# Kernel tuning notes

Measured on AMD Instinct MI355X. Metric: run time of the kernel, lower is better.

Reference implementation:

```python
import jax, jax.numpy as jnp
import numpy as np

B = 1024      # number of samples (sample_idx.shape[0])
H = 256       # hidden_size
E = 64        # number of observation events
NO = 512      # observed samples per event
D = 16        # input_size
ND = 2        # n_dim
S = 4         # euler ODE steps between consecutive events
EPS = 1e-8


def setup_inputs() -> dict:
    key = jax.random.key(0)
    ks = jax.random.split(key, 24)
    X = jax.random.normal(ks[0], (E, NO, D, ND), jnp.float32)
    M = jnp.ones((E, NO, D), jnp.float32)
    rng = np.random.default_rng(0)
    # distinct indices per event (torch scatter temp[i_obs]=... assumes no dup within event)
    batch_idx = jnp.asarray(
        np.stack([rng.permutation(B)[:NO] for _ in range(E)]).astype(np.int32))
    dt = jnp.float32(0.05)
    s = 1.0 / np.sqrt(H)
    def U(k, shp):
        return jax.random.uniform(k, shp, jnp.float32, -s, s)
    inp = {"X": X, "M": M, "batch_idx": batch_idx, "dt": dt}
    # GRU-ODE cell (3 Linear layers H->H, bias init 0.01 in torch; random here)
    inp["ode_Wr"], inp["ode_br"] = U(ks[1], (H, H)), U(ks[2], (H,))
    inp["ode_Wz"], inp["ode_bz"] = U(ks[3], (H, H)), U(ks[4], (H,))
    inp["ode_Wh"], inp["ode_bh"] = U(ks[5], (H, H)), U(ks[6], (H,))
    # GRUCell for observation update: input size 2*D, hidden H
    inp["g_Wxr"], inp["g_Wxz"], inp["g_Wxn"] = U(ks[7], (2 * D, H)), U(ks[8], (2 * D, H)), U(ks[9], (2 * D, H))
    inp["g_Uhr"], inp["g_Uhz"], inp["g_Uhn"] = U(ks[10], (H, H)), U(ks[11], (H, H)), U(ks[12], (H, H))
    inp["g_bxr"], inp["g_bxz"], inp["g_bxn"] = U(ks[13], (H,)), U(ks[14], (H,)), U(ks[15], (H,))
    inp["g_bhr"], inp["g_bhz"], inp["g_bhn"] = U(ks[16], (H,)), U(ks[17], (H,)), U(ks[18], (H,))
    # p_model: Linear(H,H) -> ReLU -> (Dropout p=0, identity in eval) -> Linear(H, D-1)
    inp["p_W1"], inp["p_b1"] = U(ks[19], (H, H)), U(ks[20], (H,))
    inp["p_W2"], inp["p_b2"] = U(ks[21], (H, D - 1)), U(ks[22], (D - 1,))
    return inp


def reference(X, M, batch_idx, dt,
              ode_Wr, ode_br, ode_Wz, ode_bz, ode_Wh, ode_bh,
              g_Wxr, g_Wxz, g_Wxn, g_Uhr, g_Uhz, g_Uhn,
              g_bxr, g_bxz, g_bxn, g_bhr, g_bhz, g_bhn,
              p_W1, p_b1, p_W2, p_b2):
    def euler_step(h):
        r = jax.nn.sigmoid(h @ ode_Wr + ode_br)
        z = jax.nn.sigmoid(h @ ode_Wz + ode_bz)
        u = jnp.tanh((r * h) @ ode_Wh + ode_bh)
        return h + dt * (1.0 - z) * (u - h)

    def event_step(carry, xs):
        h, mse, mae, mape, tot = carry
        Xe, Me, ie = xs                      # [NO,D,ND], [NO,D], [NO]
        for _ in range(S):                   # ODE evolution up to this obs time
            h = euler_step(h)
        p = jax.nn.relu(h @ p_W1 + p_b1) @ p_W2 + p_b2   # [B, D-1]
        Xt = Xe[:, 1:, 0]                    # X_obs[:, :, 0][:, 1:]
        Mt = Me[:, 1:]
        diff = Xt - p[ie]
        mse = mse + jnp.sum(diff * diff * Mt)
        mae = mae + jnp.sum(jnp.abs(diff) * Mt)
        mape = mape + jnp.sum(jnp.abs(diff) / (Xt + EPS) * Mt)
        tot = tot + jnp.sum(Mt)
        # GRUCell observation update, scattered back into h
        x_in = Xe.reshape(Xe.shape[0], -1)   # [NO, 2*D]
        hi = h[ie]                           # [NO, H]
        r = jax.nn.sigmoid(x_in @ g_Wxr + g_bxr + hi @ g_Uhr + g_bhr)
        z = jax.nn.sigmoid(x_in @ g_Wxz + g_bxz + hi @ g_Uhz + g_bhz)
        n = jnp.tanh(x_in @ g_Wxn + g_bxn + r * (hi @ g_Uhn + g_bhn))
        hn = (1.0 - z) * n + z * hi
        h = h.at[ie].set(hn)
        return (h, mse, mae, mape, tot), None

    h0 = jnp.zeros((B, H), jnp.float32)
    zero = jnp.float32(0.0)
    (h, mse, mae, mape, tot), _ = jax.lax.scan(
        event_step, (h0, zero, zero, zero, zero), (X, M, batch_idx))
    return (mse / tot, mae / tot, mape / tot)
```

## Files before the change

### kernel.cpp

```cpp
#include <hip/hip_runtime.h>

#define Bv 1024
#define Ev 64
#define NOv 512
#define L2E  1.44269504088896340736f
#define L2E2 2.88539008177792681472f

typedef _Float16 h8 __attribute__((ext_vector_type(8)));
typedef float f32x4 __attribute__((ext_vector_type(4)));
typedef int i32x8 __attribute__((ext_vector_type(8)));

#define LDH8 272
#define LDA1 264
#define LDX  48

#define MF16(a,b,c) __builtin_amdgcn_mfma_f32_16x16x32_f16((a),(b),(c),0,0,0)
#define MFS(a,b,c) __builtin_amdgcn_mfma_scale_f32_16x16x128_f8f6f4((a),(b),(c),0,0,0,0x7F7F7F7F,0,0x7F7F7F7F)

__device__ __forceinline__ float rcpf(float x) {
    float r; asm("v_rcp_f32 %0, %1" : "=v"(r) : "v"(x)); return r;
}
__device__ __forceinline__ float ex2(float x) {
    float r; asm("v_exp_f32 %0, %1" : "=v"(r) : "v"(x)); return r;
}
__device__ __forceinline__ float sig2(float y) { return rcpf(1.0f + ex2(-y)); }
__device__ __forceinline__ float tanh2(float y) { return fmaf(2.0f, sig2(y), -1.0f); }
__device__ __forceinline__ int pk4_fp8(float a, float b, float c, float d) {
    int p = __builtin_amdgcn_cvt_pk_fp8_f32(a, b, 0, false);
    p = __builtin_amdgcn_cvt_pk_fp8_f32(c, d, p, true);
    return p;
}
__device__ __forceinline__ char fp8b(float v) {
    return (char)(__builtin_amdgcn_cvt_pk_fp8_f32(v, v, 0, false) & 0xff);
}
#define GATHER(dst, A) { \
    float lo_ = sA ? A[1] : A[0]; \
    float hi_ = sA ? A[3] : A[2]; \
    dst = sB ? hi_ : lo_; }

__device__ __forceinline__ i32x8 ld8(const int4* __restrict__ A,
                                     const int4* __restrict__ B, int idx) {
    int4 lo = A[idx], hi = B[idx];
    i32x8 w;
    w[0] = lo.x; w[1] = lo.y; w[2] = lo.z; w[3] = lo.w;
    w[4] = hi.x; w[5] = hi.y; w[6] = hi.z; w[7] = hi.w;
    return w;
}

__global__ void pack_frag8w(const float* __restrict__ src, int4* __restrict__ dst,
                            int ntiles, int ncols, float scale) {
    int idx = blockIdx.x * 256 + threadIdx.x;
    int total = ntiles * 2 * 64;
    if (idx >= total) return;
    int lane = idx & 63;
    int kh = (idx >> 6) & 1;
    int ct = idx >> 7;
    int k0 = kh * 128 + (lane >> 4) * 32;
    int n = ct * 16 + (lane & 15);
    int w[8];
    #pragma unroll
    for (int q = 0; q < 8; ++q) {
        float s[4];
        #pragma unroll
        for (int j = 0; j < 4; ++j)
            s[j] = (n < ncols) ? scale * src[(k0 + q * 4 + j) * ncols + n] : 0.f;
        w[q] = pk4_fp8(s[0], s[1], s[2], s[3]);
    }
    dst[idx * 2]     = make_int4(w[0], w[1], w[2], w[3]);
    dst[idx * 2 + 1] = make_int4(w[4], w[5], w[6], w[7]);
}

__global__ void pack_frag16(const float* __restrict__ src, _Float16* __restrict__ dst,
                            int KS, int ntiles, int ncols, float scale) {
    int idx = blockIdx.x * 256 + threadIdx.x;
    int total = ntiles * KS * 64;
    if (idx >= total) return;
    int lane = idx & 63;
    int ks = (idx >> 6) % KS;
    int ct = (idx >> 6) / KS;
    int k0 = ks * 32 + (lane >> 4) * 8;
    int n = ct * 16 + (lane & 15);
    h8 v;
    #pragma unroll
    for (int j = 0; j < 8; ++j)
        v[j] = (n < ncols) ? (_Float16)(scale * src[(k0 + j) * ncols + n]) : (_Float16)0.f;
    ((h8*)dst)[idx] = v;
}

__global__ void inv_init(int* __restrict__ inv) {
    int i = blockIdx.x * blockDim.x + threadIdx.x;
    if (i < Ev * Bv) inv[i] = -1;
}
__global__ void inv_scatter(const int* __restrict__ bidx, int* __restrict__ inv) {
    int i = blockIdx.x * blockDim.x + threadIdx.x;
    if (i < Ev * NOv) {
        int e = i >> 9;
        int o = i & (NOv - 1);
        inv[e * Bv + bidx[i]] = o;
    }
}
__global__ void gather_x(const float* __restrict__ X, const int* __restrict__ bidx,
                         _Float16* __restrict__ Xg) {
    int i = blockIdx.x * 256 + threadIdx.x;
    if (i >= Ev * NOv * 32) return;
    int q = i & 31, o = (i >> 5) & (NOv - 1), e = i >> 14;
    int b = bidx[e * NOv + o];
    Xg[(e * Bv + b) * 32 + q] = (_Float16)X[i];
}
__global__ void gather_t(const float* __restrict__ X, const float* __restrict__ M,
                         const int* __restrict__ bidx,
                         float* __restrict__ Tx, float* __restrict__ Tm) {
    int i = blockIdx.x * 256 + threadIdx.x;
    if (i >= Ev * NOv * 16) return;
    int m = i & 15, o = (i >> 4) & (NOv - 1), e = i >> 13;
    int b = bidx[e * NOv + o];
    int d = (e * Bv + b) * 16 + m;
    if (m < 15) {
        Tx[d] = X[((e * NOv + o) * 16 + 1 + m) * 2];
        Tm[d] = M[(e * NOv + o) * 16 + 1 + m];
    } else {
        Tx[d] = 1.f;
        Tm[d] = 0.f;
    }
}

__global__ __launch_bounds__(1024) void gruode_main(
    const _Float16* __restrict__ Xg, const float* __restrict__ Tx, const float* __restrict__ Tm,
    const float* __restrict__ dtp,
    const float* __restrict__ br, const float* __restrict__ bz, const float* __restrict__ bh,
    const float* __restrict__ bxr, const float* __restrict__ bxz, const float* __restrict__ bxn,
    const float* __restrict__ bhr, const float* __restrict__ bhz, const float* __restrict__ bhn,
    const float* __restrict__ b1, const float* __restrict__ b2,
    const i32x8* __restrict__ WrQ, const i32x8* __restrict__ WzQ, const i32x8* __restrict__ WhQ,
    const i32x8* __restrict__ UhrQ, const i32x8* __restrict__ UhzQ, const i32x8* __restrict__ UhnQ,
    const i32x8* __restrict__ W1Q,
    const h8* __restrict__ WxrH, const h8* __restrict__ WxzH, const h8* __restrict__ WxnH,
    const h8* __restrict__ W2H,
    const int* __restrict__ inv, double* __restrict__ partials)
{
    __shared__ __align__(16) int4     UhrA[2048], UhrB[2048];
    __shared__ __align__(16) int4     UhzA[2048], UhzB[2048];
    __shared__ __align__(16) h8       W2L[512];
    __shared__ __align__(16) char     hb2[2][4 * LDH8];
    __shared__ __align__(16) _Float16 a1s[4 * LDA1];
    __shared__ __align__(16) _Float16 x16d[2][4 * LDX];
    __shared__ __align__(16) float    bias_s[5][256];
    __shared__ __align__(16) float    b2s[16];
    __shared__ int    obsi2[2][16];
    __shared__ double wred[16][4];

    const int tid  = threadIdx.x;
    const int lane = tid & 63;
    const int wid  = tid >> 6;
    const int l16  = lane & 15;
    const int lg   = lane >> 4;
    const int n0   = wid * 16 + lg * 4;
    const int row0 = blockIdx.x * 4;
    const float dtv = dtp[0];
    const int rrow = l16 & 3;

    const int rho = lane & 3;
    const int kap = lane >> 2;
    const int gam = wid * 16 + kap;
    const int hoff = rho * LDH8 + gam;
    const bool sA = (kap & 1) != 0;
    const bool sB = (kap & 2) != 0;
    const int sbase = 64 * lg + 4 * rrow;

    if (tid < 256) {
        bias_s[0][tid] = (bxr[tid] + bhr[tid]) * L2E;
        bias_s[1][tid] = (bxz[tid] + bhz[tid]) * L2E;
        bias_s[2][tid] = bxn[tid] * L2E2;
    } else if (tid < 512) {
        int t = tid - 256;
        bias_s[3][t] = bhn[t] * L2E2;
        bias_s[4][t] = b1[t];
    }
    if (tid < 16) b2s[tid] = (tid < 15) ? b2[tid] : 0.f;
    if (tid < LDH8) {
        ((int*)hb2[0])[tid] = 0;
        ((int*)hb2[1])[tid] = 0;
    }
    for (int i = tid; i < 2048; i += 1024) {
        const int4* s1 = (const int4*)&UhrQ[i];
        UhrA[i] = s1[0]; UhrB[i] = s1[1];
        const int4* s2 = (const int4*)&UhzQ[i];
        UhzA[i] = s2[0]; UhzB[i] = s2[1];
    }
    if (tid < 512) W2L[tid] = W2H[tid];
    if (tid < 16) obsi2[0][tid] = (tid < 4) ? inv[row0 + tid] : -1;
    if (tid < 128) {
        int row = tid >> 5, q = tid & 31;
        x16d[0][row * LDX + q] = Xg[(row0 + row) * 32 + q];
    }

    const float bRs = br[gam] * L2E;
    const float bZs = bz[gam] * L2E;
    const float bUs = bh[gam] * L2E2;

    i32x8 wr0 = WrQ[(wid * 2 + 0) * 64 + lane], wr1 = WrQ[(wid * 2 + 1) * 64 + lane];
    i32x8 wz0 = WzQ[(wid * 2 + 0) * 64 + lane], wz1 = WzQ[(wid * 2 + 1) * 64 + lane];
    i32x8 wh0 = WhQ[(wid * 2 + 0) * 64 + lane], wh1 = WhQ[(wid * 2 + 1) * 64 + lane];

    float hs = 0.f;
    double am0 = 0.0, am1 = 0.0, am2 = 0.0, am3 = 0.0;
    const f32x4 zf = {0.f, 0.f, 0.f, 0.f};
    __syncthreads();

    #pragma unroll 1
    for (int e = 0; e < Ev; ++e) {
        char* __restrict__ HB = hb2[e & 1];
        char* __restrict__ RB = hb2[(e & 1) ^ 1];
        const _Float16* __restrict__ xs = x16d[e & 1];
        const int* __restrict__ obs = obsi2[e & 1];

        float zs = 0.f;
        for (int s = 0; s < 4; ++s) {
            f32x4 aR = zf, aZ = zf;
            {
                i32x8 hb = *(const i32x8*)&HB[rrow * LDH8 + lg * 32];
                aR = MFS(wr0, hb, aR); aZ = MFS(wz0, hb, aZ);
                hb = *(const i32x8*)&HB[rrow * LDH8 + 128 + lg * 32];
                aR = MFS(wr1, hb, aR); aZ = MFS(wz1, hb, aZ);
            }
            float rpre, zpre;
            GATHER(rpre, aR);
            GATHER(zpre, aZ);
            float rv = sig2(rpre + bRs);
            zs = sig2(zpre + bZs);
            RB[hoff] = fp8b(rv * hs);
            __syncthreads();
            f32x4 aU = zf;
            {
                i32x8 rb = *(const i32x8*)&RB[rrow * LDH8 + lg * 32];
                aU = MFS(wh0, rb, aU);
                rb = *(const i32x8*)&RB[rrow * LDH8 + 128 + lg * 32];
                aU = MFS(wh1, rb, aU);
            }
            float upre;
            GATHER(upre, aU);
            float u = tanh2(upre + bUs);
            hs = hs + dtv * (1.f - zs) * (u - hs);
            HB[hoff] = fp8b(hs);
            __syncthreads();
        }
        __builtin_amdgcn_sched_barrier(0);

        i32x8 hb0 = *(const i32x8*)&HB[rrow * LDH8 + lg * 32];
        i32x8 hb1 = *(const i32x8*)&HB[rrow * LDH8 + 128 + lg * 32];
        f32x4 aN = *(const f32x4*)&bias_s[3][n0];
        {
            f32x4 aW = *(const f32x4*)&bias_s[4][n0];
            aN = MFS(UhnQ[(wid * 2 + 0) * 64 + lane], hb0, aN);
            aW = MFS(W1Q[(wid * 2 + 0) * 64 + lane], hb0, aW);
            aN = MFS(UhnQ[(wid * 2 + 1) * 64 + lane], hb1, aN);
            aW = MFS(W1Q[(wid * 2 + 1) * 64 + lane], hb1, aW);
            if (l16 < 4) {
                _Float16 a1v[4];
                #pragma unroll
                for (int r = 0; r < 4; ++r)
                    a1v[r] = (_Float16)fmaxf(aW[r], 0.f);
                *(long*)&a1s[l16 * LDA1 + n0] = *(const long*)a1v;
            }
        }
        {
            int en = (e + 1 < Ev) ? e + 1 : e;
            int nb = (e + 1) & 1;
            if (tid < 16) obsi2[nb][tid] = (tid < 4) ? inv[en * Bv + row0 + tid] : -1;
            if (tid < 128) {
                int row = tid >> 5, q = tid & 31;
                x16d[nb][row * LDX + q] = Xg[(en * Bv + row0 + row) * 32 + q];
            }
        }
        float4 txv = {0.f,0.f,0.f,0.f}, tmv = {0.f,0.f,0.f,0.f};
        if (wid == 0) {
            int gr = row0 + l16; if (gr > Bv - 1) gr = Bv - 1;
            txv = *(const float4*)&Tx[(e * Bv + gr) * 16 + lg * 4];
            tmv = *(const float4*)&Tm[(e * Bv + gr) * 16 + lg * 4];
        }
        float rg[4];
        {
            f32x4 aG = *(const f32x4*)&bias_s[0][n0];
            aG = MFS(ld8(UhrA, UhrB, (wid * 2 + 0) * 64 + lane), hb0, aG);
            aG = MFS(ld8(UhrA, UhrB, (wid * 2 + 1) * 64 + lane), hb1, aG);
            h8 bx = *(const h8*)&xs[rrow * LDX + lg * 8];
            aG = MF16(WxrH[wid * 64 + lane], bx, aG);
            #pragma unroll
            for (int r = 0; r < 4; ++r)
                rg[r] = sig2(aG[r]);
        }
        {
            f32x4 aG = *(const f32x4*)&bias_s[1][n0];
            aG = MFS(ld8(UhzA, UhzB, (wid * 2 + 0) * 64 + lane), hb0, aG);
            aG = MFS(ld8(UhzA, UhzB, (wid * 2 + 1) * 64 + lane), hb1, aG);
            h8 bx = *(const h8*)&xs[rrow * LDX + lg * 8];
            aG = MF16(WxzH[wid * 64 + lane], bx, aG);
            f32x4 aNx = *(const f32x4*)&bias_s[2][n0];
            aNx = MF16(WxnH[wid * 64 + lane], bx, aNx);
            float how[4];
            #pragma unroll
            for (int r = 0; r < 4; ++r)
                how[r] = __int_as_float(__builtin_amdgcn_ds_bpermute(sbase + 16 * r, __float_as_int(hs)));
            float hn[4];
            #pragma unroll
            for (int r = 0; r < 4; ++r) {
                float zg = sig2(aG[r]);
                float nv = tanh2(aNx[r] + rg[r] * aN[r]);
                hn[r] = (1.f - zg) * nv + zg * how[r];
            }
            float hng;
            GATHER(hng, hn);
            if (obs[rho] >= 0) hs = hng;
            RB[hoff] = fp8b(hs);
        }
        __syncthreads();
        if (wid == 0) {
            f32x4 aP = *(const f32x4*)&b2s[lg * 4];
            f32x4 aQ = zf;
            #pragma unroll
            for (int ks = 0; ks < 4; ++ks) {
                h8 ba = *(const h8*)&a1s[rrow * LDA1 + (2 * ks) * 32 + lg * 8];
                aP = MF16(W2L[(2 * ks) * 64 + lane], ba, aP);
                h8 bb = *(const h8*)&a1s[rrow * LDA1 + (2 * ks + 1) * 32 + lg * 8];
                aQ = MF16(W2L[(2 * ks + 1) * 64 + lane], bb, aQ);
            }
            if (obs[l16] >= 0) {
                float m0 = 0.f, m1 = 0.f, m2 = 0.f, m3 = 0.f;
                #pragma unroll
                for (int r = 0; r < 4; ++r) {
                    float p  = aP[r] + aQ[r];
                    float xt = ((const float*)&txv)[r];
                    float mt = ((const float*)&tmv)[r];
                    float diff = xt - p;
                    m0 += diff * diff * mt;
                    m1 += fabsf(diff) * mt;
                    m2 += fabsf(diff) * rcpf(xt + 1e-8f) * mt;
                    m3 += mt;
                }
                am0 += (double)m0;
                am1 += (double)m1;
                am2 += (double)m2;
                am3 += (double)m3;
            }
        }
    }

    __syncthreads();
    double v[4] = {am0, am1, am2, am3};
    #pragma unroll
    for (int m = 0; m < 4; ++m) {
        double t = v[m];
        for (int off = 32; off; off >>= 1) t += __shfl_down(t, off);
        if (lane == 0) wred[wid][m] = t;
    }
    __syncthreads();
    if (tid == 0) {
        for (int m = 0; m < 4; ++m) {
            double t = 0.0;
            for (int w = 0; w < 16; ++w) t += wred[w][m];
            partials[blockIdx.x * 4 + m] = t;
        }
    }
}

__global__ void finalize_k(const double* __restrict__ partials, float* __restrict__ out) {
    __shared__ double sd[4][4];
    int t = threadIdx.x;
    int l = t & 63, w = t >> 6;
    double v0 = partials[t * 4 + 0];
    double v1 = partials[t * 4 + 1];
    double v2 = partials[t * 4 + 2];
    double v3 = partials[t * 4 + 3];
    for (int off = 32; off; off >>= 1) {
        v0 += __shfl_down(v0, off);
        v1 += __shfl_down(v1, off);
        v2 += __shfl_down(v2, off);
        v3 += __shfl_down(v3, off);
    }
    if (l == 0) { sd[w][0] = v0; sd[w][1] = v1; sd[w][2] = v2; sd[w][3] = v3; }
    __syncthreads();
    if (t == 0) {
        double r0 = 0, r1 = 0, r2 = 0, r3 = 0;
        for (int i = 0; i < 4; ++i) { r0 += sd[i][0]; r1 += sd[i][1]; r2 += sd[i][2]; r3 += sd[i][3]; }
        out[0] = (float)(r0 / r3);
        out[1] = (float)(r1 / r3);
        out[2] = (float)(r2 / r3);
    }
}

extern "C" void kernel_launch(void* const* d_in, const int* in_sizes, int n_in,
                              void* d_out, int out_size, void* d_ws, size_t ws_size,
                              hipStream_t stream) {
    const float* X   = (const float*)d_in[0];
    const float* M   = (const float*)d_in[1];
    const int*  bidx = (const int*)d_in[2];
    const float* dtp = (const float*)d_in[3];
    const float* Wr  = (const float*)d_in[4];
    const float* brr = (const float*)d_in[5];
    const float* Wz  = (const float*)d_in[6];
    const float* bzz = (const float*)d_in[7];
    const float* Wh  = (const float*)d_in[8];
    const float* bhh = (const float*)d_in[9];
    const float* Wxr = (const float*)d_in[10];
    const float* Wxz = (const float*)d_in[11];
    const float* Wxn = (const float*)d_in[12];
    const float* Uhr = (const float*)d_in[13];
    const float* Uhz = (const float*)d_in[14];
    const float* Uhn = (const float*)d_in[15];
    const float* bxr = (const float*)d_in[16];
    const float* bxz = (const float*)d_in[17];
    const float* bxn = (const float*)d_in[18];
    const float* bhr = (const float*)d_in[19];
    const float* bhz = (const float*)d_in[20];
    const float* bhn = (const float*)d_in[21];
    const float* W1  = (const float*)d_in[22];
    const float* b1  = (const float*)d_in[23];
    const float* W2  = (const float*)d_in[24];
    const float* b2  = (const float*)d_in[25];

    char* w = (char*)d_ws;
    i32x8* WrQ  = (i32x8*)(w + 0 * 65536);
    i32x8* WzQ  = (i32x8*)(w + 1 * 65536);
    i32x8* WhQ  = (i32x8*)(w + 2 * 65536);
    i32x8* UhrQ = (i32x8*)(w + 3 * 65536);
    i32x8* UhzQ = (i32x8*)(w + 4 * 65536);
    i32x8* UhnQ = (i32x8*)(w + 5 * 65536);
    i32x8* W1Q  = (i32x8*)(w + 6 * 65536);
    _Float16* WxrH = (_Float16*)(w + 458752);
    _Float16* WxzH = (_Float16*)(w + 475136);
    _Float16* WxnH = (_Float16*)(w + 491520);
    _Float16* W2H  = (_Float16*)(w + 507904);
    int* inv = (int*)(w + 516096);
    _Float16* Xg = (_Float16*)(w + 778240);
    float* Tx = (float*)(w + 4972544);
    float* Tm = (float*)(w + 9166848);
    double* partials = (double*)(w + 13361152);

    pack_frag8w<<<8, 256, 0, stream>>>(Wr,  (int4*)WrQ,  16, 256, L2E);
    pack_frag8w<<<8, 256, 0, stream>>>(Wz,  (int4*)WzQ,  16, 256, L2E);
    pack_frag8w<<<8, 256, 0, stream>>>(Wh,  (int4*)WhQ,  16, 256, L2E2);
    pack_frag8w<<<8, 256, 0, stream>>>(Uhr, (int4*)UhrQ, 16, 256, L2E);
    pack_frag8w<<<8, 256, 0, stream>>>(Uhz, (int4*)UhzQ, 16, 256, L2E);
    pack_frag8w<<<8, 256, 0, stream>>>(Uhn, (int4*)UhnQ, 16, 256, L2E2);
    pack_frag8w<<<8, 256, 0, stream>>>(W1,  (int4*)W1Q,  16, 256, 1.0f);
    pack_frag16<<<4, 256, 0, stream>>>(Wxr, WxrH, 1, 16, 256, L2E);
    pack_frag16<<<4, 256, 0, stream>>>(Wxz, WxzH, 1, 16, 256, L2E);
    pack_frag16<<<4, 256, 0, stream>>>(Wxn, WxnH, 1, 16, 256, L2E2);
    pack_frag16<<<2, 256, 0, stream>>>(W2,  W2H,  8, 1, 15, 1.0f);
    inv_init<<<256, 256, 0, stream>>>(inv);
    inv_scatter<<<128, 256, 0, stream>>>(bidx, inv);
    gather_x<<<4096, 256, 0, stream>>>(X, bidx, Xg);
    gather_t<<<2048, 256, 0, stream>>>(X, M, bidx, Tx, Tm);

    gruode_main<<<256, 1024, 0, stream>>>(Xg, Tx, Tm, dtp,
        brr, bzz, bhh, bxr, bxz, bxn, bhr, bhz, bhn, b1, b2,
        WrQ, WzQ, WhQ, UhrQ, UhzQ, UhnQ, W1Q,
        (const h8*)WxrH, (const h8*)WxzH, (const h8*)WxnH, (const h8*)W2H,
        inv, partials);

    finalize_k<<<1, 256, 0, stream>>>(partials, (float*)d_out);
}
```

Baseline: 523.5 us.

## Swap LDS-resident weights to Uhn/W1, split Euler MFMA chains, move prefetch threads

```diff
diff --git a/kernel.cpp b/kernel.cpp
--- a/kernel.cpp
+++ b/kernel.cpp
@@ -138,8 +138,8 @@
     const h8* __restrict__ W2H,
     const int* __restrict__ inv, double* __restrict__ partials)
 {
-    __shared__ __align__(16) int4     UhrA[2048], UhrB[2048];
-    __shared__ __align__(16) int4     UhzA[2048], UhzB[2048];
+    __shared__ __align__(16) int4     UhnA[2048], UhnB[2048];
+    __shared__ __align__(16) int4     W1A[2048],  W1B[2048];
     __shared__ __align__(16) h8       W2L[512];
     __shared__ __align__(16) char     hb2[2][4 * LDH8];
     __shared__ __align__(16) _Float16 a1s[4 * LDA1];
@@ -182,10 +182,10 @@
         ((int*)hb2[1])[tid] = 0;
     }
     for (int i = tid; i < 2048; i += 1024) {
-        const int4* s1 = (const int4*)&UhrQ[i];
-        UhrA[i] = s1[0]; UhrB[i] = s1[1];
-        const int4* s2 = (const int4*)&UhzQ[i];
-        UhzA[i] = s2[0]; UhzB[i] = s2[1];
+        const int4* s1 = (const int4*)&UhnQ[i];
+        UhnA[i] = s1[0]; UhnB[i] = s1[1];
+        const int4* s2 = (const int4*)&W1Q[i];
+        W1A[i] = s2[0]; W1B[i] = s2[1];
     }
     if (tid < 512) W2L[tid] = W2H[tid];
     if (tid < 16) obsi2[0][tid] = (tid < 4) ? inv[row0 + tid] : -1;
@@ -230,16 +230,17 @@
             zs = sig2(zpre + bZs);
             RB[hoff] = fp8b(rv * hs);
             __syncthreads();
-            f32x4 aU = zf;
+            f32x4 aU0 = zf, aU1 = zf;
             {
                 i32x8 rb = *(const i32x8*)&RB[rrow * LDH8 + lg * 32];
-                aU = MFS(wh0, rb, aU);
+                aU0 = MFS(wh0, rb, aU0);
                 rb = *(const i32x8*)&RB[rrow * LDH8 + 128 + lg * 32];
-                aU = MFS(wh1, rb, aU);
-            }
-            float upre;
-            GATHER(upre, aU);
-            float u = tanh2(upre + bUs);
+                aU1 = MFS(wh1, rb, aU1);
+            }
+            float u0, u1;
+            GATHER(u0, aU0);
+            GATHER(u1, aU1);
+            float u = tanh2(u0 + u1 + bUs);
             hs = hs + dtv * (1.f - zs) * (u - hs);
             HB[hoff] = fp8b(hs);
             __syncthreads();
@@ -251,10 +252,10 @@
         f32x4 aN = *(const f32x4*)&bias_s[3][n0];
         {
             f32x4 aW = *(const f32x4*)&bias_s[4][n0];
-            aN = MFS(UhnQ[(wid * 2 + 0) * 64 + lane], hb0, aN);
-            aW = MFS(W1Q[(wid * 2 + 0) * 64 + lane], hb0, aW);
-            aN = MFS(UhnQ[(wid * 2 + 1) * 64 + lane], hb1, aN);
-            aW = MFS(W1Q[(wid * 2 + 1) * 64 + lane], hb1, aW);
+            aN = MFS(ld8(UhnA, UhnB, (wid * 2 + 0) * 64 + lane), hb0, aN);
+            aW = MFS(ld8(W1A,  W1B,  (wid * 2 + 0) * 64 + lane), hb0, aW);
+            aN = MFS(ld8(UhnA, UhnB, (wid * 2 + 1) * 64 + lane), hb1, aN);
+            aW = MFS(ld8(W1A,  W1B,  (wid * 2 + 1) * 64 + lane), hb1, aW);
             if (l16 < 4) {
                 _Float16 a1v[4];
                 #pragma unroll
@@ -266,9 +267,13 @@
         {
             int en = (e + 1 < Ev) ? e + 1 : e;
             int nb = (e + 1) & 1;
-            if (tid < 16) obsi2[nb][tid] = (tid < 4) ? inv[en * Bv + row0 + tid] : -1;
-            if (tid < 128) {
-                int row = tid >> 5, q = tid & 31;
+            if (tid >= 1008) {
+                int t = tid - 1008;
+                obsi2[nb][t] = (t < 4) ? inv[en * Bv + row0 + t] : -1;
+            }
+            if (tid >= 832 && tid < 960) {
+                int t = tid - 832;
+                int row = t >> 5, q = t & 31;
                 x16d[nb][row * LDX + q] = Xg[(en * Bv + row0 + row) * 32 + q];
             }
         }
@@ -281,8 +286,8 @@
         float rg[4];
         {
             f32x4 aG = *(const f32x4*)&bias_s[0][n0];
-            aG = MFS(ld8(UhrA, UhrB, (wid * 2 + 0) * 64 + lane), hb0, aG);
-            aG = MFS(ld8(UhrA, UhrB, (wid * 2 + 1) * 64 + lane), hb1, aG);
+            aG = MFS(UhrQ[(wid * 2 + 0) * 64 + lane], hb0, aG);
+            aG = MFS(UhrQ[(wid * 2 + 1) * 64 + lane], hb1, aG);
             h8 bx = *(const h8*)&xs[rrow * LDX + lg * 8];
             aG = MF16(WxrH[wid * 64 + lane], bx, aG);
             #pragma unroll
@@ -291,8 +296,8 @@
         }
         {
             f32x4 aG = *(const f32x4*)&bias_s[1][n0];
-            aG = MFS(ld8(UhzA, UhzB, (wid * 2 + 0) * 64 + lane), hb0, aG);
-            aG = MFS(ld8(UhzA, UhzB, (wid * 2 + 1) * 64 + lane), hb1, aG);
+            aG = MFS(UhzQ[(wid * 2 + 0) * 64 + lane], hb0, aG);
+            aG = MFS(UhzQ[(wid * 2 + 1) * 64 + lane], hb1, aG);
             h8 bx = *(const h8*)&xs[rrow * LDX + lg * 8];
             aG = MF16(WxzH[wid * 64 + lane], bx, aG);
             f32x4 aNx = *(const f32x4*)&bias_s[2][n0];
```

Result: slower. 673.1 us (+28.6%).
